# Performance work log

Measured on AMD Instinct MI355X. Metric: run time of the kernel, lower is better.

The kernel has to match this reference:

```python
import jax, jax.numpy as jnp
import numpy as np

B, T, C = 8, 2048, 1024
DK = 64  # d_k = n_embd // n_head = 1024 // 16


def setup_inputs() -> dict:
    key = jax.random.key(0)
    ks = jax.random.split(key, 4)
    X = jax.random.normal(ks[0], (B, T, C), dtype=jnp.float32)
    scale = 1.0 / np.sqrt(C)
    Wq = jax.random.normal(ks[1], (C, DK), dtype=jnp.float32) * scale
    Wk = jax.random.normal(ks[2], (C, DK), dtype=jnp.float32) * scale
    Wv = jax.random.normal(ks[3], (C, DK), dtype=jnp.float32) * scale
    bq = jnp.zeros((DK,), dtype=jnp.float32)
    bk = jnp.zeros((DK,), dtype=jnp.float32)
    bv = jnp.zeros((DK,), dtype=jnp.float32)
    return {"X": X, "Wq": Wq, "bq": bq, "Wk": Wk, "bk": bk, "Wv": Wv, "bv": bv}


def reference(X, Wq, bq, Wk, bk, Wv, bv):
    # Single-head causal self-attention (dropout disabled / eval mode).
    T_ = X.shape[1]
    Q = X @ Wq + bq  # [B, T, d_k]
    K = X @ Wk + bk
    V = X @ Wv + bv
    scores = jnp.einsum('btd,bsd->bts', Q, K) / jnp.sqrt(jnp.float32(Q.shape[-1]))
    causal = jnp.tril(jnp.ones((T_, T_), dtype=bool))  # tril mask
    scores = jnp.where(causal, scores, -jnp.inf)
    weights = jax.nn.softmax(scores, axis=-1)
    out = jnp.einsum('bts,bsd->btd', weights, V)  # [B, T, d_k]
    return out
```

## Files before the change

### kernel.cpp

```cpp
#include <hip/hip_runtime.h>
#include <math.h>

#define NB 8
#define NT 2048
#define NC 1024
#define DK 64
#define BT (NB*NT)

#define QKV_BYTES  (3u * BT * DK * 2u)
#define SLOT_BYTES 8704u

typedef unsigned short ushort_t;
typedef unsigned int uint_t;
typedef __attribute__((ext_vector_type(8))) short short8;
typedef __attribute__((ext_vector_type(4))) float f32x4;

__device__ __forceinline__ float bf2f(uint_t u) {
    union { uint_t i; float f; } v;
    v.i = u << 16;
    return v.f;
}
__device__ __forceinline__ ushort_t f2bf(float f) {
    union { float f; uint_t i; } v; v.f = f;
    uint_t x = v.i;
    return (ushort_t)((x + 0x7fffu + ((x >> 16) & 1u)) >> 16);
}
__device__ __forceinline__ uint_t pack2bf(float lo, float hi) {
    return (uint_t)f2bf(lo) | ((uint_t)f2bf(hi) << 16);
}

__device__ __forceinline__ int seg_prefix(int qt) {
    const int a = qt >> 2;
    return 2 * a * (a + 1) - 4 + (qt & 3) * (a + 1);
}

__global__ __launch_bounds__(256) void wt_prep_kernel(
    const float* __restrict__ Wq, const float* __restrict__ Wk,
    const float* __restrict__ Wv, ushort_t* __restrict__ WtG)
{
    const int tg = blockIdx.x * 256 + threadIdx.x;
    const int n  = tg >> 7;
    const int k0 = (tg & 127) * 8;
    const float* W = (n < 64) ? Wq : (n < 128) ? Wk : Wv;
    const int nc = n & 63;
    ushort_t o[8];
    #pragma unroll
    for (int j = 0; j < 8; ++j) o[j] = f2bf(W[(size_t)(k0 + j) * DK + nc]);
    *reinterpret_cast<uint4*>(&WtG[n * NC + k0]) = *reinterpret_cast<uint4*>(o);
}

__global__ __launch_bounds__(512, 4) void qkv_mfma_kernel(
    const float* __restrict__ X, const ushort_t* __restrict__ WtG,
    const float* __restrict__ bq, const float* __restrict__ bk,
    const float* __restrict__ bv, ushort_t* __restrict__ QKV)
{
    __shared__ ushort_t Xs[2][2][32 * 72];
    __shared__ float    Racc[32 * 196];
    __shared__ ushort_t VtL[64 * 40];

    const int t    = threadIdx.x;
    const int grp  = t >> 8;
    const int tg   = t & 255;
    const int w    = (t >> 6) & 3;
    const int lane = t & 63;
    const int g    = lane >> 4;
    const int col  = lane & 15;
    const int m0   = blockIdx.x * 32;
    const int kb   = grp * 512;

    const int xrow = tg >> 3;
    const int xc   = (tg & 7) * 8;

    float xf[8];
    short8 wA[6], wB[6];

    auto LOADX = [&](int k0) {
        const float4* xp = reinterpret_cast<const float4*>(
            &X[(size_t)(m0 + xrow) * NC + kb + k0 + xc]);
        float4 v0 = xp[0], v1 = xp[1];
        xf[0] = v0.x; xf[1] = v0.y; xf[2] = v0.z; xf[3] = v0.w;
        xf[4] = v1.x; xf[5] = v1.y; xf[6] = v1.z; xf[7] = v1.w;
    };
    auto LOADW = [&](int k0, short8* wn) {
        #pragma unroll
        for (int tj = 0; tj < 3; ++tj) {
            const int ng = 48 * w + 16 * tj + col;
            #pragma unroll
            for (int c = 0; c < 2; ++c)
                wn[tj * 2 + c] = *reinterpret_cast<const short8*>(
                    &WtG[ng * NC + kb + k0 + 32 * c + 8 * g]);
        }
    };
    auto WRITEX = [&](int b) {
        ushort_t xb[8];
        #pragma unroll
        for (int j = 0; j < 8; ++j) xb[j] = f2bf(xf[j]);
        *reinterpret_cast<uint4*>(&Xs[grp][b][xrow * 72 + xc]) =
            *reinterpret_cast<uint4*>(xb);
    };

    f32x4 acc[2][3];
    #pragma unroll
    for (int ri = 0; ri < 2; ++ri)
        #pragma unroll
        for (int tj = 0; tj < 3; ++tj) acc[ri][tj] = (f32x4){0.f, 0.f, 0.f, 0.f};

    auto COMPUTE = [&](int cur, short8* wc) {
        const ushort_t* XsB = Xs[grp][cur];
        #pragma unroll
        for (int c = 0; c < 2; ++c) {
            short8 af[2];
            #pragma unroll
            for (int ri = 0; ri < 2; ++ri)
                af[ri] = *reinterpret_cast<const short8*>(
                    &XsB[(16 * ri + col) * 72 + 32 * c + 8 * g]);
            #pragma unroll
            for (int ri = 0; ri < 2; ++ri)
                #pragma unroll
                for (int tj = 0; tj < 3; ++tj)
                    acc[ri][tj] = __builtin_amdgcn_mfma_f32_16x16x32_bf16(
                        af[ri], wc[tj * 2 + c], acc[ri][tj], 0, 0, 0);
        }
    };

    LOADX(0);
    LOADW(0, wA);
    WRITEX(0);

    #pragma unroll
    for (int ks2 = 0; ks2 < 4; ++ks2) {
        {
            const int ks = 2 * ks2;
            if (ks < 7) { LOADX((ks + 1) * 64); LOADW((ks + 1) * 64, wB); }
            __syncthreads();
            COMPUTE(0, wA);
            if (ks < 7) WRITEX(1);
        }
        {
            const int ks = 2 * ks2 + 1;
            if (ks < 7) { LOADX((ks + 1) * 64); LOADW((ks + 1) * 64, wA); }
            __syncthreads();
            COMPUTE(1, wB);
            if (ks < 7) WRITEX(0);
        }
    }

    __syncthreads();
    if (grp == 1) {
        #pragma unroll
        for (int ri = 0; ri < 2; ++ri)
            #pragma unroll
            for (int tj = 0; tj < 3; ++tj)
                #pragma unroll
                for (int r = 0; r < 4; ++r)
                    Racc[(16 * ri + 4 * g + r) * 196 + 48 * w + 16 * tj + col] =
                        acc[ri][tj][r];
    }
    __syncthreads();
    if (grp == 0) {
        #pragma unroll
        for (int ri = 0; ri < 2; ++ri)
            #pragma unroll
            for (int tj = 0; tj < 3; ++tj)
                #pragma unroll
                for (int r = 0; r < 4; ++r)
                    acc[ri][tj][r] +=
                        Racc[(16 * ri + 4 * g + r) * 196 + 48 * w + 16 * tj + col];

        #pragma unroll
        for (int tj = 0; tj < 3; ++tj) {
            const int ng    = 48 * w + 16 * tj + col;
            const int which = ng >> 6, ncol = ng & 63;
            const float* bp = (which == 0) ? bq : (which == 1) ? bk : bv;
            const float bb  = bp[ncol];
            if (which == 2) {
                #pragma unroll
                for (int ri = 0; ri < 2; ++ri)
                    #pragma unroll
                    for (int r = 0; r < 4; ++r)
                        VtL[ncol * 40 + 16 * ri + 4 * g + r] = f2bf(acc[ri][tj][r] + bb);
            } else {
                const float qs = (which == 0) ? 0.125f : 1.0f;
                ushort_t* Y = QKV + (size_t)which * BT * DK;
                #pragma unroll
                for (int ri = 0; ri < 2; ++ri)
                    #pragma unroll
                    for (int r = 0; r < 4; ++r) {
                        const int rowg = m0 + 16 * ri + 4 * g + r;
                        Y[(size_t)rowg * DK + ncol] = f2bf((acc[ri][tj][r] + bb) * qs);
                    }
            }
        }
    }
    __syncthreads();
    if (grp == 0) {
        ushort_t* Vt = QKV + (size_t)2 * BT * DK;
        const int d  = tg >> 2;
        const int sg = tg & 3;
        uint4 v = *reinterpret_cast<const uint4*>(&VtL[d * 40 + sg * 8]);
        *reinterpret_cast<uint4*>(&Vt[(size_t)d * BT + m0 + sg * 8]) = v;
    }
}

__global__ __launch_bounds__(256) void attn_seg_kernel(
    const ushort_t* __restrict__ QKV, float* __restrict__ Out,
    char* __restrict__ Pbase)
{
    const ushort_t* Qw = QKV;
    const ushort_t* Kw = QKV + (size_t)BT * DK;
    const ushort_t* Vw = QKV + (size_t)2 * BT * DK;

    __shared__ ushort_t Ks[256 * 72];
    __shared__ ushort_t VtL[64 * 288];

    const int t     = threadIdx.x;
    const int w     = t >> 6;
    const int lane  = t & 63;
    const int g     = lane >> 4;
    const int col   = lane & 15;
    const int batch = blockIdx.x & 7;
    const int u     = blockIdx.x >> 3;

    int s;
    if      (u < 16) s = 0;
    else if (u < 30) s = 1;
    else if (u < 42) s = 2;
    else if (u < 52) s = 3;
    else if (u < 60) s = 4;
    else if (u < 66) s = 5;
    else if (u < 70) s = 6;
    else             s = 7;
    const int off2 = 16 * s - s * (s - 1);
    const int qt0  = 4 * s + 2 * (u - off2);
    const int kbase = 256 * s;
    const int diag0 = qt0 - 4 * s;
    const int ntile = min(4, diag0 + 2);

    {
        const int sr = t >> 2;
        const int ss = t & 3;
        for (int i = 0; i < ntile; ++i) {
            const int krow = 64 * i + sr;
            const size_t gk = ((size_t)(batch * NT) + kbase + krow) * DK + ss * 16;
            const uint4* kp = reinterpret_cast<const uint4*>(Kw + gk);
            *reinterpret_cast<uint4*>(&Ks[krow * 72 + ss * 16])     = kp[0];
            *reinterpret_cast<uint4*>(&Ks[krow * 72 + ss * 16 + 8]) = kp[1];
            const size_t gv = (size_t)sr * BT + (batch * NT + kbase + 64 * i) + ss * 16;
            const uint4* vp = reinterpret_cast<const uint4*>(Vw + gv);
            *reinterpret_cast<uint4*>(&VtL[sr * 288 + 72 * i + ss * 16])     = vp[0];
            *reinterpret_cast<uint4*>(&VtL[sr * 288 + 72 * i + ss * 16 + 8]) = vp[1];
        }
    }
    __syncthreads();

    const int qrow0 = qt0 * 64 + 16 * w + col;
    const int qrow1 = qrow0 + 64;

    short8 q0a, q0b, q1a, q1b;
    {
        const ushort_t* Qr0 = Qw + ((size_t)(batch * NT) + qrow0) * DK;
        q0a = *reinterpret_cast<const short8*>(Qr0 + 8 * g);
        q0b = *reinterpret_cast<const short8*>(Qr0 + 32 + 8 * g);
        const ushort_t* Qr1 = Qw + ((size_t)(batch * NT) + qrow1) * DK;
        q1a = *reinterpret_cast<const short8*>(Qr1 + 8 * g);
        q1b = *reinterpret_cast<const short8*>(Qr1 + 32 + 8 * g);
    }

    f32x4 Oa0[4], Oa1[4];
    #pragma unroll
    for (int dt = 0; dt < 4; ++dt) {
        Oa0[dt] = (f32x4){0.f, 0.f, 0.f, 0.f};
        Oa1[dt] = (f32x4){0.f, 0.f, 0.f, 0.f};
    }
    float m0 = -INFINITY, l0 = 0.0f;
    float m1 = -INFINITY, l1 = 0.0f;

    for (int ktl = 0; ktl < ntile; ++ktl) {
        f32x4 sa0[4], sa1[4];
        #pragma unroll
        for (int tj = 0; tj < 4; ++tj) {
            sa0[tj] = (f32x4){0.f, 0.f, 0.f, 0.f};
            sa1[tj] = (f32x4){0.f, 0.f, 0.f, 0.f};
        }
        __builtin_amdgcn_s_setprio(1);
        #pragma unroll
        for (int tj = 0; tj < 4; ++tj) {
            const ushort_t* kb = &Ks[(64 * ktl + col + 16 * tj) * 72 + 8 * g];
            short8 kf0 = *reinterpret_cast<const short8*>(kb);
            short8 kf1 = *reinterpret_cast<const short8*>(kb + 32);
            sa0[tj] = __builtin_amdgcn_mfma_f32_16x16x32_bf16(kf0, q0a, sa0[tj], 0, 0, 0);
            sa0[tj] = __builtin_amdgcn_mfma_f32_16x16x32_bf16(kf1, q0b, sa0[tj], 0, 0, 0);
            sa1[tj] = __builtin_amdgcn_mfma_f32_16x16x32_bf16(kf0, q1a, sa1[tj], 0, 0, 0);
            sa1[tj] = __builtin_amdgcn_mfma_f32_16x16x32_bf16(kf1, q1b, sa1[tj], 0, 0, 0);
        }
        __builtin_amdgcn_s_setprio(0);

        const int s0 = kbase + 64 * ktl;
        if (ktl >= diag0) {
            #pragma unroll
            for (int tj = 0; tj < 4; ++tj)
                #pragma unroll
                for (int r = 0; r < 4; ++r)
                    if (s0 + 16 * tj + 4 * g + r > qrow0) sa0[tj][r] = -INFINITY;
        }
        if (ktl >= diag0 + 1) {
            #pragma unroll
            for (int tj = 0; tj < 4; ++tj)
                #pragma unroll
                for (int r = 0; r < 4; ++r)
                    if (s0 + 16 * tj + 4 * g + r > qrow1) sa1[tj][r] = -INFINITY;
        }

        float vx0 = sa0[0][0], vx1 = sa1[0][0];
        #pragma unroll
        for (int tj = 0; tj < 4; ++tj)
            #pragma unroll
            for (int r = 0; r < 4; ++r) {
                vx0 = fmaxf(vx0, sa0[tj][r]);
                vx1 = fmaxf(vx1, sa1[tj][r]);
            }
        vx0 = fmaxf(vx0, __shfl_xor(vx0, 16, 64));
        vx1 = fmaxf(vx1, __shfl_xor(vx1, 16, 64));
        vx0 = fmaxf(vx0, __shfl_xor(vx0, 32, 64));
        vx1 = fmaxf(vx1, __shfl_xor(vx1, 32, 64));

        const float mn0 = fmaxf(m0, vx0);
        const float mn1 = fmaxf(m1, vx1);
        const float sc0 = __expf(m0 - mn0);
        const float sc1 = __expf(m1 - mn1);
        m0 = mn0; m1 = mn1;

        float lt0 = 0.f, lt1 = 0.f;
        #pragma unroll
        for (int tj = 0; tj < 4; ++tj)
            #pragma unroll
            for (int r = 0; r < 4; ++r) {
                sa0[tj][r] = __expf(sa0[tj][r] - mn0);
                sa1[tj][r] = __expf(sa1[tj][r] - mn1);
                lt0 += sa0[tj][r];
                lt1 += sa1[tj][r];
            }
        lt0 += __shfl_xor(lt0, 16, 64);
        lt1 += __shfl_xor(lt1, 16, 64);
        lt0 += __shfl_xor(lt0, 32, 64);
        lt1 += __shfl_xor(lt1, 32, 64);
        l0 = l0 * sc0 + lt0;
        l1 = l1 * sc1 + lt1;

        float sco0[4], sco1[4];
        #pragma unroll
        for (int r = 0; r < 4; ++r) {
            sco0[r] = __shfl(sc0, 20 * g + r, 64);
            sco1[r] = __shfl(sc1, 20 * g + r, 64);
        }
        #pragma unroll
        for (int dt = 0; dt < 4; ++dt)
            #pragma unroll
            for (int r = 0; r < 4; ++r) {
                Oa0[dt][r] *= sco0[r];
                Oa1[dt][r] *= sco1[r];
            }

        uint_t pk00[4], pk01[4], pk10[4], pk11[4];
        #pragma unroll
        for (int tj = 0; tj < 4; ++tj) {
            pk00[tj] = pack2bf(sa0[tj][0], sa0[tj][1]);
            pk01[tj] = pack2bf(sa0[tj][2], sa0[tj][3]);
            pk10[tj] = pack2bf(sa1[tj][0], sa1[tj][1]);
            pk11[tj] = pack2bf(sa1[tj][2], sa1[tj][3]);
        }
        const int sA = col + 32 * (g & 1);
        const int sB = sA + 16;
        const bool hi = (g >= 2);

        #pragma unroll
        for (int c = 0; c < 2; ++c) {
            uint_t a0 = __shfl(pk00[2*c], sA, 64), b0 = __shfl(pk00[2*c+1], sA, 64);
            uint_t a1 = __shfl(pk01[2*c], sA, 64), b1 = __shfl(pk01[2*c+1], sA, 64);
            uint_t a2 = __shfl(pk00[2*c], sB, 64), b2 = __shfl(pk00[2*c+1], sB, 64);
            uint_t a3 = __shfl(pk01[2*c], sB, 64), b3 = __shfl(pk01[2*c+1], sB, 64);
            uint_t c0 = __shfl(pk10[2*c], sA, 64), d0 = __shfl(pk10[2*c+1], sA, 64);
            uint_t c1 = __shfl(pk11[2*c], sA, 64), d1 = __shfl(pk11[2*c+1], sA, 64);
            uint_t c2 = __shfl(pk10[2*c], sB, 64), d2 = __shfl(pk10[2*c+1], sB, 64);
            uint_t c3 = __shfl(pk11[2*c], sB, 64), d3 = __shfl(pk11[2*c+1], sB, 64);
            uint_t pa0[4], pa1[4];
            pa0[0] = hi ? b0 : a0;
            pa0[1] = hi ? b1 : a1;
            pa0[2] = hi ? b2 : a2;
            pa0[3] = hi ? b3 : a3;
            pa1[0] = hi ? d0 : c0;
            pa1[1] = hi ? d1 : c1;
            pa1[2] = hi ? d2 : c2;
            pa1[3] = hi ? d3 : c3;
            short8 paf0 = *reinterpret_cast<const short8*>(pa0);
            short8 paf1 = *reinterpret_cast<const short8*>(pa1);
            __builtin_amdgcn_s_setprio(1);
            #pragma unroll
            for (int dt = 0; dt < 4; ++dt) {
                short8 vf = *reinterpret_cast<const short8*>(
                    &VtL[(col + 16 * dt) * 288 + 72 * ktl + 32 * c + 8 * g]);
                Oa0[dt] = __builtin_amdgcn_mfma_f32_16x16x32_bf16(paf0, vf, Oa0[dt], 0, 0, 0);
                Oa1[dt] = __builtin_amdgcn_mfma_f32_16x16x32_bf16(paf1, vf, Oa1[dt], 0, 0, 0);
            }
            __builtin_amdgcn_s_setprio(0);
        }
    }

    #pragma unroll
    for (int iq = 0; iq < 2; ++iq) {
        const int qt = qt0 + iq;
        const float mm = iq ? m1 : m0;
        const float ll = iq ? l1 : l0;
        const f32x4* Oa = iq ? Oa1 : Oa0;

        float lr[4];
        #pragma unroll
        for (int r = 0; r < 4; ++r) lr[r] = __shfl(ll, 20 * g + r, 64);

        if (qt < 4) {
            #pragma unroll
            for (int r = 0; r < 4; ++r) {
                const float inv = 1.0f / lr[r];
                const int row = qt * 64 + 16 * w + 4 * g + r;
                float* op = Out + ((size_t)(batch * NT) + row) * DK + col;
                #pragma unroll
                for (int dt = 0; dt < 4; ++dt) op[16 * dt] = Oa[dt][r] * inv;
            }
        } else {
            float mr[4];
            #pragma unroll
            for (int r = 0; r < 4; ++r) mr[r] = __shfl(mm, 20 * g + r, 64);
            const int slot = batch * 140 + seg_prefix(qt) + s;
            char* sp = Pbase + (size_t)slot * SLOT_BYTES;
            ushort_t* Ob  = reinterpret_cast<ushort_t*>(sp);
            float*    Pm  = reinterpret_cast<float*>(sp + 8192);
            float*    Plv = reinterpret_cast<float*>(sp + 8448);
            #pragma unroll
            for (int r = 0; r < 4; ++r) {
                const int rloc = 16 * w + 4 * g + r;
                #pragma unroll
                for (int dt = 0; dt < 4; ++dt)
                    Ob[rloc * 64 + 16 * dt + col] = f2bf(Oa[dt][r]);
                if (col == 0) { Pm[rloc] = mr[r]; Plv[rloc] = lr[r]; }
            }
        }
    }
}

__global__ __launch_bounds__(256) void attn_combine_kernel(
    const char* __restrict__ Pbase, float* __restrict__ Out)
{
    const int bid   = blockIdx.x;
    const int batch = bid / 28;
    const int qt    = 4 + bid % 28;
    const int nseg  = (qt >> 2) + 1;
    const int slot0 = batch * 140 + seg_prefix(qt);

    const int t   = threadIdx.x;
    const int row = t >> 2;
    const int d0  = (t & 3) * 16;

    float ms[8], ls[8];
    float M = -INFINITY;
    #pragma unroll
    for (int s = 0; s < 8; ++s)
        if (s < nseg) {
            const char* sp = Pbase + (size_t)(slot0 + s) * SLOT_BYTES;
            ms[s] = reinterpret_cast<const float*>(sp + 8192)[row];
            ls[s] = reinterpret_cast<const float*>(sp + 8448)[row];
            M = fmaxf(M, ms[s]);
        }

    float acc[16];
    #pragma unroll
    for (int j = 0; j < 16; ++j) acc[j] = 0.f;
    float ltot = 0.f;

    #pragma unroll
    for (int s = 0; s < 8; ++s)
        if (s < nseg) {
            const float wsc = __expf(ms[s] - M);
            ltot += wsc * ls[s];
            const ushort_t* Ob = reinterpret_cast<const ushort_t*>(
                Pbase + (size_t)(slot0 + s) * SLOT_BYTES) + row * 64 + d0;
            uint4 u0 = *reinterpret_cast<const uint4*>(Ob);
            uint4 u1 = *reinterpret_cast<const uint4*>(Ob + 8);
            const uint_t* uu = reinterpret_cast<const uint_t*>(&u0);
            #pragma unroll
            for (int j = 0; j < 4; ++j) {
                acc[2*j+0] += wsc * bf2f(uu[j] & 0xffffu);
                acc[2*j+1] += wsc * bf2f(uu[j] >> 16);
            }
            const uint_t* uv = reinterpret_cast<const uint_t*>(&u1);
            #pragma unroll
            for (int j = 0; j < 4; ++j) {
                acc[8+2*j+0] += wsc * bf2f(uv[j] & 0xffffu);
                acc[8+2*j+1] += wsc * bf2f(uv[j] >> 16);
            }
        }

    const float inv = 1.0f / ltot;
    float* op = Out + ((size_t)(batch * NT) + qt * 64 + row) * DK + d0;
    #pragma unroll
    for (int j = 0; j < 16; ++j) op[j] = acc[j] * inv;
}

extern "C" void kernel_launch(void* const* d_in, const int* in_sizes, int n_in,
                              void* d_out, int out_size, void* d_ws, size_t ws_size,
                              hipStream_t stream) {
    const float* X  = (const float*)d_in[0];
    const float* Wq = (const float*)d_in[1];
    const float* bq = (const float*)d_in[2];
    const float* Wk = (const float*)d_in[3];
    const float* bk = (const float*)d_in[4];
    const float* Wv = (const float*)d_in[5];
    const float* bv = (const float*)d_in[6];
    float* Out = (float*)d_out;
    ushort_t* QKV = (ushort_t*)d_ws;
    char* Pbase   = (char*)d_ws + QKV_BYTES;
    ushort_t* WtG = (ushort_t*)d_out;

    wt_prep_kernel<<<96, 256, 0, stream>>>(Wq, Wk, Wv, WtG);
    qkv_mfma_kernel<<<512, 512, 0, stream>>>(X, WtG, bq, bk, bv, QKV);
    attn_seg_kernel<<<576, 256, 0, stream>>>(QKV, Out, Pbase);
    attn_combine_kernel<<<224, 256, 0, stream>>>(Pbase, Out);
}
```

Baseline: 66.17 us.

## Fuse split-K combine into attention kernel via last-arriver atomic counters

Removes the separate combine kernel launch. Each attention block increments a per-query-tile atomic counter after writing its partial results, and the last segment to finish merges all partials and writes the final output. The counters are zeroed in the weight-prep kernel. This saves one launch and the gap between kernels, at the cost of threadfences, atomics, and tail work added to the last-arriving blocks.

```diff
diff --git a/kernel.cpp b/kernel.cpp
--- a/kernel.cpp
+++ b/kernel.cpp
@@ -9,6 +9,8 @@
 
 #define QKV_BYTES  (3u * BT * DK * 2u)
 #define SLOT_BYTES 8704u
+#define NSLOTS     1120u
+#define NCNT       224
 
 typedef unsigned short ushort_t;
 typedef unsigned int uint_t;
@@ -36,8 +38,10 @@
 
 __global__ __launch_bounds__(256) void wt_prep_kernel(
     const float* __restrict__ Wq, const float* __restrict__ Wk,
-    const float* __restrict__ Wv, ushort_t* __restrict__ WtG)
+    const float* __restrict__ Wv, ushort_t* __restrict__ WtG,
+    int* __restrict__ Cnt)
 {
+    if (blockIdx.x == 0 && threadIdx.x < NCNT) Cnt[threadIdx.x] = 0;
     const int tg = blockIdx.x * 256 + threadIdx.x;
     const int n  = tg >> 7;
     const int k0 = (tg & 127) * 8;
@@ -204,7 +208,7 @@
 
 __global__ __launch_bounds__(256) void attn_seg_kernel(
     const ushort_t* __restrict__ QKV, float* __restrict__ Out,
-    char* __restrict__ Pbase)
+    char* __restrict__ Pbase, int* __restrict__ Cnt)
 {
     const ushort_t* Qw = QKV;
     const ushort_t* Kw = QKV + (size_t)BT * DK;
@@ -212,6 +216,7 @@
 
     __shared__ ushort_t Ks[256 * 72];
     __shared__ ushort_t VtL[64 * 288];
+    __shared__ int s_old[2];
 
     const int t     = threadIdx.x;
     const int w     = t >> 6;
@@ -445,64 +450,68 @@
             }
         }
     }
-}
-
-__global__ __launch_bounds__(256) void attn_combine_kernel(
-    const char* __restrict__ Pbase, float* __restrict__ Out)
-{
-    const int bid   = blockIdx.x;
-    const int batch = bid / 28;
-    const int qt    = 4 + bid % 28;
-    const int nseg  = (qt >> 2) + 1;
-    const int slot0 = batch * 140 + seg_prefix(qt);
-
-    const int t   = threadIdx.x;
-    const int row = t >> 2;
-    const int d0  = (t & 3) * 16;
-
-    float ms[8], ls[8];
-    float M = -INFINITY;
-    #pragma unroll
-    for (int s = 0; s < 8; ++s)
-        if (s < nseg) {
-            const char* sp = Pbase + (size_t)(slot0 + s) * SLOT_BYTES;
-            ms[s] = reinterpret_cast<const float*>(sp + 8192)[row];
-            ls[s] = reinterpret_cast<const float*>(sp + 8448)[row];
-            M = fmaxf(M, ms[s]);
-        }
-
-    float acc[16];
-    #pragma unroll
-    for (int j = 0; j < 16; ++j) acc[j] = 0.f;
-    float ltot = 0.f;
-
-    #pragma unroll
-    for (int s = 0; s < 8; ++s)
-        if (s < nseg) {
-            const float wsc = __expf(ms[s] - M);
-            ltot += wsc * ls[s];
-            const ushort_t* Ob = reinterpret_cast<const ushort_t*>(
-                Pbase + (size_t)(slot0 + s) * SLOT_BYTES) + row * 64 + d0;
-            uint4 u0 = *reinterpret_cast<const uint4*>(Ob);
-            uint4 u1 = *reinterpret_cast<const uint4*>(Ob + 8);
-            const uint_t* uu = reinterpret_cast<const uint_t*>(&u0);
-            #pragma unroll
-            for (int j = 0; j < 4; ++j) {
-                acc[2*j+0] += wsc * bf2f(uu[j] & 0xffffu);
-                acc[2*j+1] += wsc * bf2f(uu[j] >> 16);
-            }
-            const uint_t* uv = reinterpret_cast<const uint_t*>(&u1);
-            #pragma unroll
-            for (int j = 0; j < 4; ++j) {
-                acc[8+2*j+0] += wsc * bf2f(uv[j] & 0xffffu);
-                acc[8+2*j+1] += wsc * bf2f(uv[j] >> 16);
-            }
-        }
-
-    const float inv = 1.0f / ltot;
-    float* op = Out + ((size_t)(batch * NT) + qt * 64 + row) * DK + d0;
-    #pragma unroll
-    for (int j = 0; j < 16; ++j) op[j] = acc[j] * inv;
+
+    if (qt0 >= 4) {
+        __threadfence();
+        if (t < 2) s_old[t] = atomicAdd(&Cnt[batch * 28 + (qt0 + t - 4)], 1);
+        __syncthreads();
+        const int nsegq = (qt0 >> 2) + 1;
+
+        #pragma unroll
+        for (int iq = 0; iq < 2; ++iq) {
+            if (s_old[iq] == nsegq - 1) {
+                __threadfence();
+                const int qt    = qt0 + iq;
+                const int slot0 = batch * 140 + seg_prefix(qt);
+                const int row   = t >> 2;
+                const int d0    = (t & 3) * 16;
+
+                float ms[8], ls[8];
+                float M = -INFINITY;
+                #pragma unroll
+                for (int s2 = 0; s2 < 8; ++s2)
+                    if (s2 < nsegq) {
+                        const char* sp = Pbase + (size_t)(slot0 + s2) * SLOT_BYTES;
+                        ms[s2] = reinterpret_cast<const float*>(sp + 8192)[row];
+                        ls[s2] = reinterpret_cast<const float*>(sp + 8448)[row];
+                        M = fmaxf(M, ms[s2]);
+                    }
+
+                float acc[16];
+                #pragma unroll
+                for (int j = 0; j < 16; ++j) acc[j] = 0.f;
+                float ltot = 0.f;
+
+                #pragma unroll
+                for (int s2 = 0; s2 < 8; ++s2)
+                    if (s2 < nsegq) {
+                        const float wsc = __expf(ms[s2] - M);
+                        ltot += wsc * ls[s2];
+                        const ushort_t* Ob = reinterpret_cast<const ushort_t*>(
+                            Pbase + (size_t)(slot0 + s2) * SLOT_BYTES) + row * 64 + d0;
+                        uint4 u0 = *reinterpret_cast<const uint4*>(Ob);
+                        uint4 u1 = *reinterpret_cast<const uint4*>(Ob + 8);
+                        const uint_t* uu = reinterpret_cast<const uint_t*>(&u0);
+                        #pragma unroll
+                        for (int j = 0; j < 4; ++j) {
+                            acc[2*j+0] += wsc * bf2f(uu[j] & 0xffffu);
+                            acc[2*j+1] += wsc * bf2f(uu[j] >> 16);
+                        }
+                        const uint_t* uv = reinterpret_cast<const uint_t*>(&u1);
+                        #pragma unroll
+                        for (int j = 0; j < 4; ++j) {
+                            acc[8+2*j+0] += wsc * bf2f(uv[j] & 0xffffu);
+                            acc[8+2*j+1] += wsc * bf2f(uv[j] >> 16);
+                        }
+                    }
+
+                const float inv = 1.0f / ltot;
+                float* op = Out + ((size_t)(batch * NT) + qt * 64 + row) * DK + d0;
+                #pragma unroll
+                for (int j = 0; j < 16; ++j) op[j] = acc[j] * inv;
+            }
+        }
+    }
 }
 
 extern "C" void kernel_launch(void* const* d_in, const int* in_sizes, int n_in,
@@ -518,10 +527,10 @@
     float* Out = (float*)d_out;
     ushort_t* QKV = (ushort_t*)d_ws;
     char* Pbase   = (char*)d_ws + QKV_BYTES;
+    int* Cnt      = (int*)(Pbase + (size_t)NSLOTS * SLOT_BYTES);
     ushort_t* WtG = (ushort_t*)d_out;
 
-    wt_prep_kernel<<<96, 256, 0, stream>>>(Wq, Wk, Wv, WtG);
+    wt_prep_kernel<<<96, 256, 0, stream>>>(Wq, Wk, Wv, WtG, Cnt);
     qkv_mfma_kernel<<<512, 512, 0, stream>>>(X, WtG, bq, bk, bv, QKV);
-    attn_seg_kernel<<<576, 256, 0, stream>>>(QKV, Out, Pbase);
-    attn_combine_kernel<<<224, 256, 0, stream>>>(Pbase, Out);
-}
+    attn_seg_kernel<<<576, 256, 0, stream>>>(QKV, Out, Pbase, Cnt);
+}
```

Result: slower. 161.1 us (+143.4%).
